# Optimization experiments

Measured on AMD Instinct MI355X. Metric: run time of the kernel, lower is better.

Reference implementation:

```python
import jax, jax.numpy as jnp
import numpy as np

N_NODES = 100000
N_EDGES = 3200000
IN_DIM = 128
H_GCN = 64
H_LSTM = 64


def setup_inputs() -> dict:
    key = jax.random.key(0)
    ks = jax.random.split(key, 12)
    s = 0.05
    return {
        "x": jax.random.normal(ks[0], (IN_DIM, N_NODES), dtype=jnp.float32),
        "edge_index": jax.random.randint(ks[1], (2, N_EDGES), 0, N_NODES, dtype=jnp.int32),
        "W1": jax.random.normal(ks[2], (IN_DIM, H_GCN), dtype=jnp.float32) * s,
        "b1": jnp.zeros((H_GCN,), dtype=jnp.float32),
        "W2": jax.random.normal(ks[3], (H_GCN, H_GCN), dtype=jnp.float32) * s,
        "b2": jnp.zeros((H_GCN,), dtype=jnp.float32),
        "w_ih": jax.random.normal(ks[4], (4 * H_LSTM, H_GCN), dtype=jnp.float32) * s,
        "w_hh": jax.random.normal(ks[5], (4 * H_LSTM, H_LSTM), dtype=jnp.float32) * s,
        "b_ih": jax.random.normal(ks[6], (4 * H_LSTM,), dtype=jnp.float32) * s,
        "b_hh": jax.random.normal(ks[7], (4 * H_LSTM,), dtype=jnp.float32) * s,
        "fc_w": jax.random.normal(ks[8], (1, H_LSTM), dtype=jnp.float32) * s,
        "fc_b": jnp.zeros((1,), dtype=jnp.float32),
    }


def gcn_conv(x, src, dst, n, W, b):
    # PyG GCNConv: add self loops, symmetric norm D^-1/2 (A+I) D^-1/2, linear-first.
    h = x @ W  # [N, out]
    loop = jnp.arange(n, dtype=src.dtype)
    s = jnp.concatenate([src, loop])
    d = jnp.concatenate([dst, loop])
    deg = jax.ops.segment_sum(jnp.ones(d.shape, dtype=h.dtype), d, num_segments=n)
    dinv = jnp.where(deg > 0, jax.lax.rsqrt(deg), 0.0)
    norm = dinv[s] * dinv[d]  # [E+N]
    out = jax.ops.segment_sum(h[s] * norm[:, None], d, num_segments=n)
    return out + b


def reference(x, edge_index, W1, b1, W2, b2, w_ih, w_hh, b_ih, b_hh, fc_w, fc_b):
    xt = x.T  # data.x.T -> [N, input_dim]
    n = xt.shape[0]
    src, dst = edge_index[0], edge_index[1]
    h = jax.nn.relu(gcn_conv(xt, src, dst, n, W1, b1))
    h = gcn_conv(h, src, dst, n, W2, b2)
    z = h[0][None, :]  # [1, H_GCN] node 0 embedding
    # single-step LSTM, zero initial state (h0=c0=0)
    gates = z @ w_ih.T + b_ih + b_hh  # [1, 4H]
    i, f, g, o = jnp.split(gates, 4, axis=-1)
    c = jax.nn.sigmoid(i) * jnp.tanh(g)  # f*c0 = 0
    hy = jax.nn.sigmoid(o) * jnp.tanh(c)  # [1, H_LSTM]
    y = hy @ fc_w.T + fc_b  # [1, 1]
    return y[:, :, None]  # [1, 1, 1]
```

## Files before the change

### kernel.cpp

```cpp
#include <hip/hip_runtime.h>
#include <math.h>

#define N_NODES 100000
#define N_EDGES 3200000
#define IN_DIM 128
#define HG 64

#define E0CAP 2048
#define MCAP  65536
#define NBMW  3125
#define SCAN_BLOCKS 1024
#define BLK_E0 16

#define OFF_DEG       0u
#define OFF_SLOTMAP   400000u
#define OFF_CNT       800000u
#define OFF_ACC       800032u
#define OFF_BMS1      1324320u
#define OFF_BMNEED    1336864u
#define WS_ZERO_BYTES 1349408u
#define OFF_BCNT      1349408u
#define OFF_BLIST     1353504u
#define OFF_EDGES0    1419040u
#define OFF_SLOTNODE  1427232u
#define OFF_MLIST     1435424u

__device__ __forceinline__ float dinv_of(int degv) {
    return 1.0f / sqrtf((float)(degv + 1));
}

__global__ void k_scan0(const int* __restrict__ src, const int* __restrict__ dst,
                        int4* __restrict__ zbase, int* __restrict__ bcnt,
                        int* __restrict__ blist) {
    __shared__ int lcnt;
    __shared__ int lsrc[BLK_E0];
    if (threadIdx.x == 0) lcnt = 0;
    __syncthreads();
    int tid = blockIdx.x * blockDim.x + threadIdx.x;
    int nth = gridDim.x * blockDim.x;
    const int nz = WS_ZERO_BYTES / 16;
    int4 z; z.x = 0; z.y = 0; z.z = 0; z.w = 0;
    for (int i = tid; i < nz; i += nth) zbase[i] = z;
    const int4* dst4 = (const int4*)dst;
    const int n4 = N_EDGES / 4;
    for (int i = tid; i < n4; i += nth) {
        int4 dv = dst4[i];
        int ds[4] = {dv.x, dv.y, dv.z, dv.w};
#pragma unroll
        for (int k = 0; k < 4; k++) {
            if (ds[k] == 0) {
                int p = atomicAdd(&lcnt, 1);
                if (p < BLK_E0) lsrc[p] = src[4 * i + k];
            }
        }
    }
    __syncthreads();
    int c = lcnt; if (c > BLK_E0) c = BLK_E0;
    if (threadIdx.x == 0) bcnt[blockIdx.x] = c;
    for (int i = threadIdx.x; i < c; i += blockDim.x)
        blist[blockIdx.x * BLK_E0 + i] = lsrc[i];
}

__global__ void k_build_slots(const int* __restrict__ bcnt, const int* __restrict__ blist,
                              int* __restrict__ edges0, int* __restrict__ slotnodes,
                              int* __restrict__ slotmap, int* __restrict__ cnt,
                              unsigned* __restrict__ bmS1) {
    const int t = threadIdx.x;
    for (int b = t; b < SCAN_BLOCKS; b += blockDim.x) {
        int c = bcnt[b];
        if (c > 0) {
            int p = atomicAdd(&cnt[0], c);
            for (int j = 0; j < c && p + j < E0CAP; j++)
                edges0[p + j] = blist[b * BLK_E0 + j];
        }
    }
    __syncthreads();
    int n0 = atomicAdd(&cnt[0], 0); if (n0 > E0CAP) n0 = E0CAP;
    for (int i = t; i < n0 + 1; i += blockDim.x) {
        int s = (i == n0) ? 0 : edges0[i];
        if (atomicCAS(&slotmap[s], 0, 1) == 0) {
            int p = atomicAdd(&cnt[1], 1);
            if (p < E0CAP) slotnodes[p] = s;
        }
    }
    __syncthreads();
    int ns = atomicAdd(&cnt[1], 0); if (ns > E0CAP) ns = E0CAP;
    for (int i = t; i < ns; i += blockDim.x) {
        int s = slotnodes[i];
        slotmap[s] = i + 1;
        atomicOr(&bmS1[s >> 5], 1u << (s & 31));
    }
}

__global__ void k_match(const int* __restrict__ src, const int* __restrict__ dst,
                        const unsigned* __restrict__ bmS1, unsigned* __restrict__ bmNeed,
                        int* __restrict__ cnt, int* __restrict__ mlist) {
    __shared__ unsigned sbm[NBMW];
    for (int i = threadIdx.x; i < NBMW; i += blockDim.x) sbm[i] = bmS1[i];
    __syncthreads();
    int tid = blockIdx.x * blockDim.x + threadIdx.x;
    int nth = gridDim.x * blockDim.x;
    const int4* dst4 = (const int4*)dst;
    const int n4 = N_EDGES / 4;
    for (int i = tid; i < n4; i += nth) {
        int4 dv = dst4[i];
        unsigned ds[4] = {(unsigned)dv.x, (unsigned)dv.y, (unsigned)dv.z, (unsigned)dv.w};
#pragma unroll
        for (int k = 0; k < 4; k++) {
            unsigned d = ds[k];
            if ((sbm[d >> 5] >> (d & 31)) & 1u) {
                int e = 4 * i + k;
                int p = atomicAdd(&cnt[2], 1);
                if (p < MCAP) mlist[p] = e;
                int s = src[e];
                atomicOr(&bmNeed[s >> 5], 1u << (s & 31));
            }
        }
    }
}

__global__ void k_deg_need(const int* __restrict__ dst, const unsigned* __restrict__ bmS1,
                           const unsigned* __restrict__ bmNeed, int* __restrict__ deg) {
    __shared__ unsigned sbm[NBMW];
    for (int i = threadIdx.x; i < NBMW; i += blockDim.x) sbm[i] = bmS1[i] | bmNeed[i];
    __syncthreads();
    int tid = blockIdx.x * blockDim.x + threadIdx.x;
    int nth = gridDim.x * blockDim.x;
    const int4* dst4 = (const int4*)dst;
    const int n4 = N_EDGES / 4;
    for (int i = tid; i < n4; i += nth) {
        int4 dv = dst4[i];
        unsigned ds[4] = {(unsigned)dv.x, (unsigned)dv.y, (unsigned)dv.z, (unsigned)dv.w};
#pragma unroll
        for (int k = 0; k < 4; k++) {
            unsigned d = ds[k];
            if ((sbm[d >> 5] >> (d & 31)) & 1u) atomicAdd(&deg[d], 1);
        }
    }
}

#define CHUNK 256
__global__ void k_contrib_final(const int* __restrict__ src, const int* __restrict__ dst,
                                const int* __restrict__ deg, const int* __restrict__ slotmap,
                                int* __restrict__ cnt, const int* __restrict__ mlist,
                                const int* __restrict__ slotnodes, const int* __restrict__ edges0,
                                const float* __restrict__ x, const float* __restrict__ W1,
                                const float* __restrict__ b1, const float* __restrict__ W2,
                                const float* __restrict__ b2, const float* __restrict__ w_ih,
                                const float* __restrict__ b_ih, const float* __restrict__ b_hh,
                                const float* __restrict__ fc_w, const float* __restrict__ fc_b,
                                float* __restrict__ acc, float* __restrict__ out) {
    int m = cnt[2]; if (m > MCAP) m = MCAP;
    int ns = cnt[1]; if (ns > E0CAP) ns = E0CAP;
    const int total = m + ns;
    const int t = threadIdx.x;
    const int j = t & 63;
    const int wk = (blockIdx.x << 2) | (t >> 6);
    const int nwk = gridDim.x << 2;
    for (int ii = wk; ii < total; ii += nwk) {
        int s, sl;
        float w;
        if (ii < m) {
            int e = mlist[ii];
            s = src[e];
            int d = dst[e];
            sl = slotmap[d] - 1;
            w = dinv_of(deg[s]) * dinv_of(deg[d]);
        } else {
            sl = ii - m;
            s = slotnodes[sl];
            float dv = dinv_of(deg[s]);
            w = dv * dv;
        }
        float g = 0.f;
#pragma unroll 8
        for (int k = 0; k < IN_DIM; k++) {
            g = fmaf(x[(size_t)k * N_NODES + s], W1[k * HG + j], g);
        }
        atomicAdd(&acc[sl * HG + j], g * w);
    }

    __syncthreads();
    __threadfence();
    __shared__ int amLast;
    if (t == 0) amLast = (atomicAdd(&cnt[3], 1) == (int)gridDim.x - 1);
    __syncthreads();
    if (!amLast) return;

    __shared__ int   sh_sl[CHUNK];
    __shared__ float sh_w[CHUNK];
    __shared__ float partial[4][HG];
    __shared__ float agg[HG];
    __shared__ float zv[HG];
    __shared__ float gates[4 * HG];
    __shared__ float hw[HG];
    const int ch = t & (HG - 1);
    const int grp = t >> 6;
    int n0 = cnt[0]; if (n0 > E0CAP) n0 = E0CAP;

    const float dinv0 = dinv_of(deg[0]);
    const float bch = b1[ch];

    float a = 0.f;
    for (int base = 0; base < n0; base += CHUNK) {
        int cn = n0 - base; if (cn > CHUNK) cn = CHUNK;
        __syncthreads();
        if (t < cn) {
            int s = edges0[base + t];
            sh_sl[t] = slotmap[s] - 1;
            sh_w[t] = dinv_of(deg[s]) * dinv0;
        }
        __syncthreads();
        for (int i = grp; i < cn; i += 4) {
            float h = atomicAdd(&acc[sh_sl[i] * HG + ch], 0.f) + bch;
            a = fmaf(sh_w[i], (h > 0.f ? h : 0.f), a);
        }
    }
    partial[grp][ch] = a;
    __syncthreads();
    if (t < HG) {
        int sl0 = slotmap[0] - 1;
        float h0 = atomicAdd(&acc[sl0 * HG + t], 0.f) + b1[t];
        float s = dinv0 * dinv0 * (h0 > 0.f ? h0 : 0.f);
        s += partial[0][t] + partial[1][t] + partial[2][t] + partial[3][t];
        agg[t] = s;
    }
    __syncthreads();

    if (t < HG) {
        float zz = b2[t];
#pragma unroll 8
        for (int k = 0; k < HG; k++) zz = fmaf(agg[k], W2[k * HG + t], zz);
        zv[t] = zz;
    }
    __syncthreads();

    {
        float gt = b_ih[t] + b_hh[t];
#pragma unroll 8
        for (int jj = 0; jj < HG; jj++) gt = fmaf(zv[jj], w_ih[t * HG + jj], gt);
        gates[t] = gt;
    }
    __syncthreads();

    if (t < HG) {
        float ig = 1.f / (1.f + expf(-gates[t]));
        float gg = tanhf(gates[2 * HG + t]);
        float og = 1.f / (1.f + expf(-gates[3 * HG + t]));
        float c = ig * gg;
        float hy = og * tanhf(c);
        hw[t] = hy * fc_w[t];
    }
    __syncthreads();
    if (t == 0) {
        float y = fc_b[0];
        for (int jj = 0; jj < HG; jj++) y += hw[jj];
        out[0] = y;
    }
}

extern "C" void kernel_launch(void* const* d_in, const int* in_sizes, int n_in,
                              void* d_out, int out_size, void* d_ws, size_t ws_size,
                              hipStream_t stream) {
    const float* x    = (const float*)d_in[0];
    const int*   ei   = (const int*)d_in[1];
    const float* W1   = (const float*)d_in[2];
    const float* b1   = (const float*)d_in[3];
    const float* W2   = (const float*)d_in[4];
    const float* b2   = (const float*)d_in[5];
    const float* w_ih = (const float*)d_in[6];
    const float* b_ih = (const float*)d_in[8];
    const float* b_hh = (const float*)d_in[9];
    const float* fc_w = (const float*)d_in[10];
    const float* fc_b = (const float*)d_in[11];
    float* out = (float*)d_out;

    const int* src = ei;
    const int* dst = ei + N_EDGES;

    char* ws = (char*)d_ws;
    int*      deg       = (int*)(ws + OFF_DEG);
    int*      slotmap   = (int*)(ws + OFF_SLOTMAP);
    int*      cnt       = (int*)(ws + OFF_CNT);
    float*    acc       = (float*)(ws + OFF_ACC);
    unsigned* bmS1      = (unsigned*)(ws + OFF_BMS1);
    unsigned* bmNeed    = (unsigned*)(ws + OFF_BMNEED);
    int*      bcnt      = (int*)(ws + OFF_BCNT);
    int*      blist     = (int*)(ws + OFF_BLIST);
    int*      edges0    = (int*)(ws + OFF_EDGES0);
    int*      slotnodes = (int*)(ws + OFF_SLOTNODE);
    int*      mlist     = (int*)(ws + OFF_MLIST);

    k_scan0<<<SCAN_BLOCKS, 256, 0, stream>>>(src, dst, (int4*)ws, bcnt, blist);
    k_build_slots<<<1, 256, 0, stream>>>(bcnt, blist, edges0, slotnodes, slotmap, cnt, bmS1);
    k_match<<<SCAN_BLOCKS, 256, 0, stream>>>(src, dst, bmS1, bmNeed, cnt, mlist);
    k_deg_need<<<SCAN_BLOCKS, 256, 0, stream>>>(dst, bmS1, bmNeed, deg);
    k_contrib_final<<<256, 256, 0, stream>>>(src, dst, deg, slotmap, cnt, mlist,
                                             slotnodes, edges0, x, W1, b1, W2, b2,
                                             w_ih, b_ih, b_hh, fc_w, fc_b, acc, out);
}
```

Baseline: 194.4 us.

## Split contrib/final kernels, pre-resolve match metadata, halve K per block

The match kernel now stores each matched edge's source, slot index and destination directly, so the contrib kernel no longer gathers src/dst/slotmap through the edge id. The contrib kernel is split from the final LSTM stage and relaunched with 4096 blocks of 64 threads, each handling half of the 128-dim K range. This exposes more parallelism for the gathered x loads. The last-block completion detection is replaced by a separate single-block final kernel, which reads acc plainly instead of through atomics. This adds one kernel launch and doubles the number of atomicAdds into acc.

```diff
diff --git a/kernel.cpp b/kernel.cpp
--- a/kernel.cpp
+++ b/kernel.cpp
@@ -23,7 +23,8 @@
 #define OFF_BLIST     1353504u
 #define OFF_EDGES0    1419040u
 #define OFF_SLOTNODE  1427232u
-#define OFF_MLIST     1435424u
+#define OFF_MLISTS    1435424u
+#define OFF_MLISTD    1697568u
 
 __device__ __forceinline__ float dinv_of(int degv) {
     return 1.0f / sqrtf((float)(degv + 1));
@@ -93,8 +94,10 @@
 }
 
 __global__ void k_match(const int* __restrict__ src, const int* __restrict__ dst,
+                        const int* __restrict__ slotmap,
                         const unsigned* __restrict__ bmS1, unsigned* __restrict__ bmNeed,
-                        int* __restrict__ cnt, int* __restrict__ mlist) {
+                        int* __restrict__ cnt, int* __restrict__ mlistS,
+                        int* __restrict__ mlistD) {
     __shared__ unsigned sbm[NBMW];
     for (int i = threadIdx.x; i < NBMW; i += blockDim.x) sbm[i] = bmS1[i];
     __syncthreads();
@@ -110,9 +113,13 @@
             unsigned d = ds[k];
             if ((sbm[d >> 5] >> (d & 31)) & 1u) {
                 int e = 4 * i + k;
+                int s = src[e];
+                int sl = slotmap[d] - 1;
                 int p = atomicAdd(&cnt[2], 1);
-                if (p < MCAP) mlist[p] = e;
-                int s = src[e];
+                if (p < MCAP) {
+                    mlistS[p] = s | (sl << 17);
+                    mlistD[p] = (int)d;
+                }
                 atomicOr(&bmNeed[s >> 5], 1u << (s & 31));
             }
         }
@@ -139,32 +146,25 @@
     }
 }
 
-#define CHUNK 256
-__global__ void k_contrib_final(const int* __restrict__ src, const int* __restrict__ dst,
-                                const int* __restrict__ deg, const int* __restrict__ slotmap,
-                                int* __restrict__ cnt, const int* __restrict__ mlist,
-                                const int* __restrict__ slotnodes, const int* __restrict__ edges0,
-                                const float* __restrict__ x, const float* __restrict__ W1,
-                                const float* __restrict__ b1, const float* __restrict__ W2,
-                                const float* __restrict__ b2, const float* __restrict__ w_ih,
-                                const float* __restrict__ b_ih, const float* __restrict__ b_hh,
-                                const float* __restrict__ fc_w, const float* __restrict__ fc_b,
-                                float* __restrict__ acc, float* __restrict__ out) {
+__global__ void k_contrib(const int* __restrict__ deg, const int* __restrict__ cnt,
+                          const int* __restrict__ mlistS, const int* __restrict__ mlistD,
+                          const int* __restrict__ slotnodes,
+                          const float* __restrict__ x, const float* __restrict__ W1,
+                          float* __restrict__ acc) {
     int m = cnt[2]; if (m > MCAP) m = MCAP;
     int ns = cnt[1]; if (ns > E0CAP) ns = E0CAP;
-    const int total = m + ns;
-    const int t = threadIdx.x;
-    const int j = t & 63;
-    const int wk = (blockIdx.x << 2) | (t >> 6);
-    const int nwk = gridDim.x << 2;
-    for (int ii = wk; ii < total; ii += nwk) {
+    const int vtotal = 2 * (m + ns);
+    const int j = threadIdx.x;
+    for (int v = blockIdx.x; v < vtotal; v += gridDim.x) {
+        const int ii = v >> 1;
+        const int kbase = (v & 1) << 6;
         int s, sl;
         float w;
         if (ii < m) {
-            int e = mlist[ii];
-            s = src[e];
-            int d = dst[e];
-            sl = slotmap[d] - 1;
+            int sw = mlistS[ii];
+            int d = mlistD[ii];
+            s = sw & 0x1FFFF;
+            sl = sw >> 17;
             w = dinv_of(deg[s]) * dinv_of(deg[d]);
         } else {
             sl = ii - m;
@@ -172,21 +172,25 @@
             float dv = dinv_of(deg[s]);
             w = dv * dv;
         }
+        const float* xp = x + (size_t)kbase * N_NODES + s;
+        const float* wp = W1 + kbase * HG + j;
         float g = 0.f;
-#pragma unroll 8
-        for (int k = 0; k < IN_DIM; k++) {
-            g = fmaf(x[(size_t)k * N_NODES + s], W1[k * HG + j], g);
+#pragma unroll
+        for (int k = 0; k < 64; k++) {
+            g = fmaf(xp[(size_t)k * N_NODES], wp[k * HG], g);
         }
         atomicAdd(&acc[sl * HG + j], g * w);
     }
-
-    __syncthreads();
-    __threadfence();
-    __shared__ int amLast;
-    if (t == 0) amLast = (atomicAdd(&cnt[3], 1) == (int)gridDim.x - 1);
-    __syncthreads();
-    if (!amLast) return;
-
+}
+
+#define CHUNK 256
+__global__ void k_final(const float* __restrict__ b1, const float* __restrict__ W2,
+                        const float* __restrict__ b2, const float* __restrict__ w_ih,
+                        const float* __restrict__ b_ih, const float* __restrict__ b_hh,
+                        const float* __restrict__ fc_w, const float* __restrict__ fc_b,
+                        const int* __restrict__ deg, const int* __restrict__ slotmap,
+                        const int* __restrict__ cnt, const int* __restrict__ edges0,
+                        const float* __restrict__ acc, float* __restrict__ out) {
     __shared__ int   sh_sl[CHUNK];
     __shared__ float sh_w[CHUNK];
     __shared__ float partial[4][HG];
@@ -194,6 +198,7 @@
     __shared__ float zv[HG];
     __shared__ float gates[4 * HG];
     __shared__ float hw[HG];
+    const int t = threadIdx.x;
     const int ch = t & (HG - 1);
     const int grp = t >> 6;
     int n0 = cnt[0]; if (n0 > E0CAP) n0 = E0CAP;
@@ -212,7 +217,7 @@
         }
         __syncthreads();
         for (int i = grp; i < cn; i += 4) {
-            float h = atomicAdd(&acc[sh_sl[i] * HG + ch], 0.f) + bch;
+            float h = acc[sh_sl[i] * HG + ch] + bch;
             a = fmaf(sh_w[i], (h > 0.f ? h : 0.f), a);
         }
     }
@@ -220,7 +225,7 @@
     __syncthreads();
     if (t < HG) {
         int sl0 = slotmap[0] - 1;
-        float h0 = atomicAdd(&acc[sl0 * HG + t], 0.f) + b1[t];
+        float h0 = acc[sl0 * HG + t] + b1[t];
         float s = dinv0 * dinv0 * (h0 > 0.f ? h0 : 0.f);
         s += partial[0][t] + partial[1][t] + partial[2][t] + partial[3][t];
         agg[t] = s;
@@ -289,13 +294,15 @@
     int*      blist     = (int*)(ws + OFF_BLIST);
     int*      edges0    = (int*)(ws + OFF_EDGES0);
     int*      slotnodes = (int*)(ws + OFF_SLOTNODE);
-    int*      mlist     = (int*)(ws + OFF_MLIST);
+    int*      mlistS    = (int*)(ws + OFF_MLISTS);
+    int*      mlistD    = (int*)(ws + OFF_MLISTD);
 
     k_scan0<<<SCAN_BLOCKS, 256, 0, stream>>>(src, dst, (int4*)ws, bcnt, blist);
     k_build_slots<<<1, 256, 0, stream>>>(bcnt, blist, edges0, slotnodes, slotmap, cnt, bmS1);
-    k_match<<<SCAN_BLOCKS, 256, 0, stream>>>(src, dst, bmS1, bmNeed, cnt, mlist);
+    k_match<<<SCAN_BLOCKS, 256, 0, stream>>>(src, dst, slotmap, bmS1, bmNeed, cnt,
+                                             mlistS, mlistD);
     k_deg_need<<<SCAN_BLOCKS, 256, 0, stream>>>(dst, bmS1, bmNeed, deg);
-    k_contrib_final<<<256, 256, 0, stream>>>(src, dst, deg, slotmap, cnt, mlist,
-                                             slotnodes, edges0, x, W1, b1, W2, b2,
-                                             w_ih, b_ih, b_hh, fc_w, fc_b, acc, out);
-}
+    k_contrib<<<4096, 64, 0, stream>>>(deg, cnt, mlistS, mlistD, slotnodes, x, W1, acc);
+    k_final<<<1, 256, 0, stream>>>(b1, W2, b2, w_ih, b_ih, b_hh, fc_w, fc_b,
+                                   deg, slotmap, cnt, edges0, acc, out);
+}
```

Result: faster. 168.8 us, median of 2 (-13.2%).
